# Performance work log

Hardware: AMD Instinct MI355X
Metric: run time of the kernel (lower is better)

The kernel has to match this reference:

```python
import jax, jax.numpy as jnp
import numpy as np

D_IN = 1024
D_OUT = 1024


def setup_inputs() -> dict:
    key = jax.random.key(0)
    kx, kq, kk, kv = jax.random.split(key, 4)
    x = jax.random.normal(kx, (4, 2048, D_IN), dtype=jnp.float32)
    s = 1.0 / np.sqrt(D_IN)
    # Linear weights stored torch-style as [d_out, d_in]
    W_q = jax.random.uniform(kq, (D_OUT, D_IN), jnp.float32, -s, s)
    W_k = jax.random.uniform(kk, (D_OUT, D_IN), jnp.float32, -s, s)
    W_v = jax.random.uniform(kv, (D_OUT, D_IN), jnp.float32, -s, s)
    return {"x": x, "W_q": W_q, "W_k": W_k, "W_v": W_v}


def reference(x, W_q, W_k, W_v):
    b, n, _ = x.shape
    q = jnp.einsum('bnd,od->bno', x, W_q)
    k = jnp.einsum('bnd,od->bno', x, W_k)
    v = jnp.einsum('bnd,od->bno', x, W_v)
    scores = jnp.einsum('bqo,bko->bqk', q, k)  # [b, n, n]
    causal = jnp.triu(jnp.ones((n, n), dtype=bool), k=1)
    scores = jnp.where(causal, -jnp.inf, scores)
    w = jax.nn.softmax(scores / jnp.sqrt(jnp.asarray(k.shape[-1], scores.dtype)), axis=-1)
    # dropout prob = 0.0 -> identity
    return jnp.einsum('bqk,bko->bqo', w, v)
```

## Files before the change

### kernel.cpp

```cpp
#include <hip/hip_runtime.h>
#include <hip/hip_bf16.h>

typedef unsigned int uint32;
typedef unsigned short ushort_t;

typedef __bf16 bf16x8 __attribute__((ext_vector_type(8)));
typedef float f32x4 __attribute__((ext_vector_type(4)));

__device__ __forceinline__ ushort_t f2bf(float f) {
    uint32 u = __float_as_uint(f);
    u += 0x7fffu + ((u >> 16) & 1u);
    return (ushort_t)(u >> 16);
}
__device__ __forceinline__ float bf2f(ushort_t h) {
    return __uint_as_float(((uint32)h) << 16);
}

union U16 { int4 v; ushort_t u[8]; };

__device__ __forceinline__ void gll16(const ushort_t* g, ushort_t* l) {
    __builtin_amdgcn_global_load_lds(
        (const __attribute__((address_space(1))) unsigned int*)g,
        (__attribute__((address_space(3))) unsigned int*)l, 16, 0, 0);
}

#define SBAR() __builtin_amdgcn_s_barrier()
#define VM0()  asm volatile("s_waitcnt vmcnt(0)" ::: "memory")
#define VM1()  asm volatile("s_waitcnt vmcnt(1)" ::: "memory")
#define VM2()  asm volatile("s_waitcnt vmcnt(2)" ::: "memory")

__device__ __forceinline__ int frag3(int r, int kk) {
    return r * 32 + ((((kk >> 3) ^ ((r >> 1) & 3))) << 3);
}

template<int NT>
__device__ __forceinline__ void gemm256_bk32(
    const ushort_t* __restrict__ A, int lda,
    const ushort_t* __restrict__ B, int ldb,
    ushort_t* lds, f32x4 acc[4][4])
{
    const int tid = threadIdx.x;
    const int lane = tid & 63, wid = tid >> 6;
    const int wm = wid >> 2, wn = wid & 3;
    const int l15 = lane & 15, kk = (lane >> 4) * 8;
    const int srow = tid >> 2;
    const int sc4 = (tid & 3) ^ ((tid >> 3) & 3);

    #define STAGE3(G, ldg, X, op)                                            \
        gll16(&(G)[(size_t)srow * (ldg) + (X) * 32 + sc4 * 8],               \
              &lds[(((X) % 3) * 2 + (op)) * 8192 + tid * 8])

    STAGE3(A, lda, 0, 0);
    STAGE3(B, ldb, 0, 1);
    if (NT > 1) { STAGE3(B, ldb, 1, 1); VM1(); } else { VM0(); }
    SBAR();

    for (int t = 0; t < NT; ++t) {
        const ushort_t* Ab = lds + (t % 3) * 16384;
        const ushort_t* Bb = Ab + 8192;
        if (t + 1 < NT) STAGE3(A, lda, t + 1, 0);
        if (t + 2 < NT) STAGE3(B, ldb, t + 2, 1);
        bf16x8 af[4], bfr[4];
#pragma unroll
        for (int m = 0; m < 4; ++m)
            af[m] = *(const bf16x8*)&Ab[frag3(wm * 64 + m * 16 + l15, kk)];
#pragma unroll
        for (int n = 0; n < 4; ++n)
            bfr[n] = *(const bf16x8*)&Bb[frag3(wn * 64 + n * 16 + l15, kk)];
#pragma unroll
        for (int m = 0; m < 4; ++m)
#pragma unroll
            for (int n = 0; n < 4; ++n)
                acc[m][n] = __builtin_amdgcn_mfma_f32_16x16x32_bf16(
                    af[m], bfr[n], acc[m][n], 0, 0, 0);
        if (t + 1 < NT) {
            if (t + 2 < NT) VM1(); else VM0();
            SBAR();
        }
    }
    #undef STAGE3
}

__device__ __forceinline__ void gemm128_bk32(
    const ushort_t* __restrict__ A, int lda,
    const ushort_t* __restrict__ B, int ldb,
    ushort_t* lds, int NT, f32x4 acc[4][4])
{
    const int tid = threadIdx.x;
    const int lane = tid & 63, wid = tid >> 6;
    const int wm = wid >> 1, wn = wid & 1;
    const int l15 = lane & 15, kk = (lane >> 4) * 8;

    #define STG128(G, ldg, X, op) do {                                       \
        _Pragma("unroll")                                                    \
        for (int i = 0; i < 2; ++i) {                                        \
            int c = i * 256 + tid;                   \
            int row = c >> 2;                                                \
            int slot = (c & 3) ^ ((row >> 1) & 3);                           \
            gll16(&(G)[(size_t)row * (ldg) + (X) * 32 + slot * 8],           \
                  &lds[(((X) % 3) * 2 + (op)) * 4096 + c * 8]);              \
        } } while (0)

    STG128(A, lda, 0, 0);
    STG128(B, ldb, 0, 1);
    if (NT > 1) { STG128(B, ldb, 1, 1); VM2(); } else { VM0(); }
    SBAR();

    for (int t = 0; t < NT; ++t) {
        const ushort_t* Ab = lds + (t % 3) * 8192;
        const ushort_t* Bb = Ab + 4096;
        if (t + 1 < NT) STG128(A, lda, t + 1, 0);
        if (t + 2 < NT) STG128(B, ldb, t + 2, 1);
        bf16x8 af[4], bfr[4];
#pragma unroll
        for (int m = 0; m < 4; ++m)
            af[m] = *(const bf16x8*)&Ab[frag3(wm * 64 + m * 16 + l15, kk)];
#pragma unroll
        for (int n = 0; n < 4; ++n)
            bfr[n] = *(const bf16x8*)&Bb[frag3(wn * 64 + n * 16 + l15, kk)];
#pragma unroll
        for (int m = 0; m < 4; ++m)
#pragma unroll
            for (int n = 0; n < 4; ++n)
                acc[m][n] = __builtin_amdgcn_mfma_f32_16x16x32_bf16(
                    af[m], bfr[n], acc[m][n], 0, 0, 0);
        if (t + 1 < NT) {
            if (t + 2 < NT) VM2(); else VM0();
            SBAR();
        }
    }
    #undef STG128
}

__global__ __launch_bounds__(256) void conv_x(
    const float* __restrict__ X, const float* __restrict__ Wv,
    ushort_t* __restrict__ Xb, ushort_t* __restrict__ BmatV)
{
    int gb = blockIdx.x;
    const float* src;
    ushort_t* dst;
    if (gb < 4096) {
        size_t base = ((size_t)gb * 256 + threadIdx.x) * 8;
        src = X + base; dst = Xb + base;
    } else {
        size_t base = ((size_t)(gb - 4096) * 256 + threadIdx.x) * 8;
        src = Wv + base; dst = BmatV + base;
    }
    float4 f0 = *(const float4*)src;
    float4 f1 = *(const float4*)(src + 4);
    U16 o;
    o.u[0] = f2bf(f0.x); o.u[1] = f2bf(f0.y); o.u[2] = f2bf(f0.z); o.u[3] = f2bf(f0.w);
    o.u[4] = f2bf(f1.x); o.u[5] = f2bf(f1.y); o.u[6] = f2bf(f1.z); o.u[7] = f2bf(f1.w);
    *(int4*)dst = o.v;
}

__global__ __launch_bounds__(256) void convT_w(
    const float* __restrict__ Wq, const float* __restrict__ Wk,
    ushort_t* __restrict__ WqT, ushort_t* __restrict__ WkT)
{
    __shared__ ushort_t ts[64][72];
    const float* W = blockIdx.z ? Wk : Wq;
    ushort_t* Dt = blockIdx.z ? WkT : WqT;
    const int o0 = blockIdx.x * 64, d0 = blockIdx.y * 64;
    const int tid = threadIdx.x;
    const int row = tid >> 2, q = tid & 3;
#pragma unroll
    for (int c4 = 0; c4 < 4; ++c4) {
        float4 f = *(const float4*)&W[(size_t)(o0 + row) * 1024 + d0 + q * 16 + c4 * 4];
        ts[row][q * 16 + c4 * 4 + 0] = f2bf(f.x);
        ts[row][q * 16 + c4 * 4 + 1] = f2bf(f.y);
        ts[row][q * 16 + c4 * 4 + 2] = f2bf(f.z);
        ts[row][q * 16 + c4 * 4 + 3] = f2bf(f.w);
    }
    __syncthreads();
#pragma unroll
    for (int i = 0; i < 2; ++i) {
        int c = tid + 256 * i;
        int drow = c >> 3, ocol8 = c & 7;
        U16 vv;
#pragma unroll
        for (int j = 0; j < 8; ++j) vv.u[j] = ts[ocol8 * 8 + j][drow];
        *(int4*)&Dt[(size_t)(d0 + drow) * 1024 + o0 + ocol8 * 8] = vv.v;
    }
}

__global__ __launch_bounds__(256) void mt_gemm(
    const ushort_t* __restrict__ WkT, const ushort_t* __restrict__ WqT,
    ushort_t* __restrict__ Bmat)
{
    __shared__ __align__(16) ushort_t lds[24576];
    const int bm = blockIdx.y, bn = blockIdx.x;
    const int tid = threadIdx.x;
    f32x4 acc[4][4] = {};
    gemm128_bk32(WkT + (size_t)bm * 128 * 1024, 1024,
                 WqT + (size_t)bn * 128 * 1024, 1024, lds, 32, acc);
    ushort_t* Dst = Bmat + (size_t)bm * 128 * 1024 + bn * 128;
    const int lane = tid & 63, wid = tid >> 6;
    const int wr = wid >> 1, wc = wid & 1;
#pragma unroll
    for (int m = 0; m < 4; ++m)
#pragma unroll
        for (int n = 0; n < 4; ++n)
#pragma unroll
            for (int j = 0; j < 4; ++j) {
                int row = wr * 64 + m * 16 + (lane >> 4) * 4 + j;
                int col = wc * 64 + n * 16 + (lane & 15);
                Dst[(size_t)row * 1024 + col] = f2bf(acc[m][n][j]);
            }
}

__global__ __launch_bounds__(1024) void t1v_gemm256(
    const ushort_t* __restrict__ Xb, const ushort_t* __restrict__ Bmat,
    ushort_t* __restrict__ T1, ushort_t* __restrict__ V)
{
    __shared__ __align__(16) ushort_t lds[49152];
    const int id = blockIdx.x;
    const int xcd = id & 7, l = id >> 3;
    const int bm = xcd * 4 + (l >> 3);
    const int bn = l & 7;
    f32x4 acc[4][4] = {};
    gemm256_bk32<32>(Xb + (size_t)bm * 256 * 1024, 1024,
                     Bmat + (size_t)bn * 256 * 1024, 1024, lds, acc);
    ushort_t* Dst = ((bn < 4) ? T1 : V)
                  + (size_t)bm * 256 * 1024 + (bn & 3) * 256;
    const int tid = threadIdx.x, lane = tid & 63, wid = tid >> 6;
    const int wm = wid >> 2, wn = wid & 3;
#pragma unroll
    for (int m = 0; m < 4; ++m)
#pragma unroll
        for (int n = 0; n < 4; ++n)
#pragma unroll
            for (int j = 0; j < 4; ++j) {
                int row = wm * 64 + m * 16 + (lane >> 4) * 4 + j;
                int col = wn * 64 + n * 16 + (lane & 15);
                Dst[(size_t)row * 1024 + col] = f2bf(acc[m][n][j]);
            }
}

__global__ __launch_bounds__(1024) void scores_gemm256(
    const ushort_t* __restrict__ T1, const ushort_t* __restrict__ Xb,
    ushort_t* __restrict__ P,
    const ushort_t* __restrict__ V, ushort_t* __restrict__ Vt)
{
    __shared__ __align__(16) ushort_t lds[49152];
    const int id = blockIdx.x;
    const int xcd = id & 7, l = id >> 3;
    const int b = xcd >> 1, h = xcd & 1;
    const int bm = 4 * h + (l >> 3);
    const int bn = l & 7;
    const int tid = threadIdx.x;
    if (bn > bm) {
        ushort_t (*ts)[72] = (ushort_t(*)[72])lds;
        const ushort_t* Vb = V + (size_t)b * 2048 * 1024;
        ushort_t* Vtb = Vt + (size_t)b * 1024 * 2048;
        const int rank = bn * (bn - 1) / 2 + bm;
        for (int t = rank; t < 512; t += 28) {
            int k0 = (t >> 4) * 64, d0 = (t & 15) * 64;
            __syncthreads();
            if (tid < 512) {
                int row = tid >> 3, col8 = tid & 7;
                U16 vv;
                vv.v = *(const int4*)&Vb[(size_t)(k0 + row) * 1024 + d0 + col8 * 8];
#pragma unroll
                for (int j = 0; j < 8; ++j) ts[row][col8 * 8 + j] = vv.u[j];
            }
            __syncthreads();
            if (tid < 512) {
                int drow = tid >> 3, kcol8 = tid & 7;
                U16 vv;
#pragma unroll
                for (int j = 0; j < 8; ++j) vv.u[j] = ts[kcol8 * 8 + j][drow];
                *(int4*)&Vtb[(size_t)(d0 + drow) * 2048 + k0 + kcol8 * 8] = vv.v;
            }
        }
        return;
    }
    f32x4 acc[4][4] = {};
    gemm256_bk32<32>(T1 + (size_t)b * 2048 * 1024 + (size_t)bm * 256 * 1024, 1024,
                     Xb + (size_t)b * 2048 * 1024 + (size_t)bn * 256 * 1024, 1024,
                     lds, acc);
    ushort_t* Pb = P + (size_t)b * 2048 * 2048 + (size_t)bm * 256 * 2048 + bn * 256;
    const int lane = tid & 63, wid = tid >> 6;
    const int wm = wid >> 2, wn = wid & 3;
#pragma unroll
    for (int m = 0; m < 4; ++m)
#pragma unroll
        for (int n = 0; n < 4; ++n)
#pragma unroll
            for (int j = 0; j < 4; ++j) {
                int row = wm * 64 + m * 16 + (lane >> 4) * 4 + j;
                int col = wn * 64 + n * 16 + (lane & 15);
                Pb[(size_t)row * 2048 + col] = f2bf(acc[m][n][j] * 0.03125f);
            }
}

__global__ __launch_bounds__(256) void softmax_rows(ushort_t* __restrict__ P)
{
    const int q = blockIdx.x, b = blockIdx.y;
    ushort_t* row = P + ((size_t)b * 2048 + q) * 2048;
    const int tid = threadIdx.x;
    const int kmax = ((q >> 7) + 1) * 128;
    const bool active = tid * 8 < kmax;
    float v[8];
    float m = -3.0e38f;
    if (active) {
        U16 in;
        in.v = *(const int4*)&row[tid * 8];
#pragma unroll
        for (int j = 0; j < 8; ++j) {
            int k = tid * 8 + j;
            float s = bf2f(in.u[j]);
            v[j] = (k <= q) ? s : -3.0e38f;
            m = fmaxf(m, v[j]);
        }
    } else {
#pragma unroll
        for (int j = 0; j < 8; ++j) v[j] = -3.0e38f;
    }
#pragma unroll
    for (int off = 32; off >= 1; off >>= 1) m = fmaxf(m, __shfl_xor(m, off));
    __shared__ float red[4];
    if ((tid & 63) == 0) red[tid >> 6] = m;
    __syncthreads();
    m = fmaxf(fmaxf(red[0], red[1]), fmaxf(red[2], red[3]));
    float e[8], s = 0.f;
#pragma unroll
    for (int j = 0; j < 8; ++j) {
        e[j] = (v[j] > -1.0e38f) ? __expf(v[j] - m) : 0.f;
        s += e[j];
    }
#pragma unroll
    for (int off = 32; off >= 1; off >>= 1) s += __shfl_xor(s, off);
    __syncthreads();
    if ((tid & 63) == 0) red[tid >> 6] = s;
    __syncthreads();
    s = red[0] + red[1] + red[2] + red[3];
    float inv = 1.f / s;
    if (active) {
        U16 outv;
#pragma unroll
        for (int j = 0; j < 8; ++j) outv.u[j] = f2bf(e[j] * inv);
        *(int4*)&row[tid * 8] = outv.v;
    }
}

__global__ __launch_bounds__(256) void pv_gemm(
    const ushort_t* __restrict__ P, const ushort_t* __restrict__ Vt,
    float* __restrict__ O)
{
    __shared__ __align__(16) ushort_t lds[24576];
    const int L = blockIdx.x;
    int b, bm, bn;
    if (L < 256) {
        int c = L >> 4;
        b = c >> 3; bn = c & 7; bm = 15 - (L & 15);
    } else {
        int L2 = L - 256;
        int c = L2 >> 4;
        b = 2 + (c >> 3); bn = c & 7; bm = L2 & 15;
    }
    const int tid = threadIdx.x;
    const ushort_t* A = P + (size_t)b * 2048 * 2048 + (size_t)bm * 128 * 2048;
    const ushort_t* Bm = Vt + (size_t)b * 1024 * 2048 + (size_t)bn * 128 * 2048;
    f32x4 acc[4][4] = {};
    const int NT = (bm + 1) * 4;
    gemm128_bk32(A, 2048, Bm, 2048, lds, NT, acc);
    float* Ob = O + (size_t)b * 2048 * 1024 + (size_t)bm * 128 * 1024 + bn * 128;
    const int lane = tid & 63, wid = tid >> 6;
    const int wr = wid >> 1, wc = wid & 1;
#pragma unroll
    for (int m = 0; m < 4; ++m)
#pragma unroll
        for (int n = 0; n < 4; ++n)
#pragma unroll
            for (int j = 0; j < 4; ++j) {
                int row = wr * 64 + m * 16 + (lane >> 4) * 4 + j;
                int col = wc * 64 + n * 16 + (lane & 15);
                Ob[(size_t)row * 1024 + col] = acc[m][n][j];
            }
}

extern "C" void kernel_launch(void* const* d_in, const int* in_sizes, int n_in,
                              void* d_out, int out_size, void* d_ws, size_t ws_size,
                              hipStream_t stream) {
    const float* x  = (const float*)d_in[0];
    const float* Wq = (const float*)d_in[1];
    const float* Wk = (const float*)d_in[2];
    const float* Wv = (const float*)d_in[3];
    float* out = (float*)d_out;
    ushort_t* ws = (ushort_t*)d_ws;
    const size_t M1 = (size_t)1024 * 1024;
    ushort_t* P    = ws;
    ushort_t* WqT  = ws;
    ushort_t* WkT  = ws + M1;
    ushort_t* Bmat = ws + 2 * M1;
    ushort_t* Xb   = ws + 16 * M1;
    ushort_t* T1   = ws + 24 * M1;
    ushort_t* V    = ws + 32 * M1;
    ushort_t* Vt   = ws + 40 * M1;

    conv_x<<<dim3(4096 + 512), 256, 0, stream>>>(x, Wv, Xb, Bmat + M1);
    convT_w<<<dim3(16, 16, 2), 256, 0, stream>>>(Wq, Wk, WqT, WkT);
    mt_gemm<<<dim3(8, 8), 256, 0, stream>>>(WkT, WqT, Bmat);
    t1v_gemm256<<<dim3(256), 1024, 0, stream>>>(Xb, Bmat, T1, V);
    scores_gemm256<<<dim3(256), 1024, 0, stream>>>(T1, Xb, P, V, Vt);
    softmax_rows<<<dim3(2048, 4), 256, 0, stream>>>(P);
    pv_gemm<<<dim3(512), 256, 0, stream>>>(P, Vt, out);
}
```

Baseline: 148.3 us.

## Fuse causal softmax into PV GEMM with online softmax and merge conversion kernels

Removes the separate softmax pass over the bf16 score matrix and applies an online softmax inside the PV GEMM. Each tile computes running row max and sum across the 16-lane fragment group, rescales accumulators when the max grows, and normalizes at the end. This saves a full read and write of the score matrix plus one launch, at the cost of extra ALU, shuffle and exp work inside the MFMA loop. The two fp32-to-bf16 conversion kernels are also merged into one launch.

```diff
diff --git a/kernel.cpp b/kernel.cpp
--- a/kernel.cpp
+++ b/kernel.cpp
@@ -17,6 +17,7 @@
 }
 
 union U16 { int4 v; ushort_t u[8]; };
+union UB8 { bf16x8 v; ushort_t u[8]; };
 
 __device__ __forceinline__ void gll16(const ushort_t* g, ushort_t* l) {
     __builtin_amdgcn_global_load_lds(
@@ -94,7 +95,7 @@
     #define STG128(G, ldg, X, op) do {                                       \
         _Pragma("unroll")                                                    \
         for (int i = 0; i < 2; ++i) {                                        \
-            int c = i * 256 + tid;                   \
+            int c = i * 256 + tid;                                           \
             int row = c >> 2;                                                \
             int slot = (c & 3) ^ ((row >> 1) & 3);                           \
             gll16(&(G)[(size_t)row * (ldg) + (X) * 32 + slot * 8],           \
@@ -132,37 +133,39 @@
     #undef STG128
 }
 
-__global__ __launch_bounds__(256) void conv_x(
-    const float* __restrict__ X, const float* __restrict__ Wv,
-    ushort_t* __restrict__ Xb, ushort_t* __restrict__ BmatV)
-{
-    int gb = blockIdx.x;
-    const float* src;
-    ushort_t* dst;
-    if (gb < 4096) {
-        size_t base = ((size_t)gb * 256 + threadIdx.x) * 8;
-        src = X + base; dst = Xb + base;
-    } else {
-        size_t base = ((size_t)(gb - 4096) * 256 + threadIdx.x) * 8;
-        src = Wv + base; dst = BmatV + base;
-    }
-    float4 f0 = *(const float4*)src;
-    float4 f1 = *(const float4*)(src + 4);
-    U16 o;
-    o.u[0] = f2bf(f0.x); o.u[1] = f2bf(f0.y); o.u[2] = f2bf(f0.z); o.u[3] = f2bf(f0.w);
-    o.u[4] = f2bf(f1.x); o.u[5] = f2bf(f1.y); o.u[6] = f2bf(f1.z); o.u[7] = f2bf(f1.w);
-    *(int4*)dst = o.v;
-}
-
-__global__ __launch_bounds__(256) void convT_w(
-    const float* __restrict__ Wq, const float* __restrict__ Wk,
+__global__ __launch_bounds__(256) void conv_all(
+    const float* __restrict__ X,  const float* __restrict__ Wq,
+    const float* __restrict__ Wk, const float* __restrict__ Wv,
+    ushort_t* __restrict__ Xb, ushort_t* __restrict__ BmatV,
     ushort_t* __restrict__ WqT, ushort_t* __restrict__ WkT)
 {
     __shared__ ushort_t ts[64][72];
-    const float* W = blockIdx.z ? Wk : Wq;
-    ushort_t* Dt = blockIdx.z ? WkT : WqT;
-    const int o0 = blockIdx.x * 64, d0 = blockIdx.y * 64;
-    const int tid = threadIdx.x;
+    const int gb = blockIdx.x;
+    const int tid = threadIdx.x;
+    if (gb < 4608) {
+        const float* src;
+        ushort_t* dst;
+        if (gb < 4096) {
+            size_t base = ((size_t)gb * 256 + tid) * 8;
+            src = X + base; dst = Xb + base;
+        } else {
+            size_t base = ((size_t)(gb - 4096) * 256 + tid) * 8;
+            src = Wv + base; dst = BmatV + base;
+        }
+        float4 f0 = *(const float4*)src;
+        float4 f1 = *(const float4*)(src + 4);
+        U16 o;
+        o.u[0] = f2bf(f0.x); o.u[1] = f2bf(f0.y); o.u[2] = f2bf(f0.z); o.u[3] = f2bf(f0.w);
+        o.u[4] = f2bf(f1.x); o.u[5] = f2bf(f1.y); o.u[6] = f2bf(f1.z); o.u[7] = f2bf(f1.w);
+        *(int4*)dst = o.v;
+        return;
+    }
+    const int t2 = gb - 4608;
+    const int z = t2 >> 8;
+    const int bx = t2 & 15, by = (t2 >> 4) & 15;
+    const float* W = z ? Wk : Wq;
+    ushort_t* Dt = z ? WkT : WqT;
+    const int o0 = bx * 64, d0 = by * 64;
     const int row = tid >> 2, q = tid & 3;
 #pragma unroll
     for (int c4 = 0; c4 < 4; ++c4) {
@@ -294,58 +297,8 @@
             }
 }
 
-__global__ __launch_bounds__(256) void softmax_rows(ushort_t* __restrict__ P)
-{
-    const int q = blockIdx.x, b = blockIdx.y;
-    ushort_t* row = P + ((size_t)b * 2048 + q) * 2048;
-    const int tid = threadIdx.x;
-    const int kmax = ((q >> 7) + 1) * 128;
-    const bool active = tid * 8 < kmax;
-    float v[8];
-    float m = -3.0e38f;
-    if (active) {
-        U16 in;
-        in.v = *(const int4*)&row[tid * 8];
-#pragma unroll
-        for (int j = 0; j < 8; ++j) {
-            int k = tid * 8 + j;
-            float s = bf2f(in.u[j]);
-            v[j] = (k <= q) ? s : -3.0e38f;
-            m = fmaxf(m, v[j]);
-        }
-    } else {
-#pragma unroll
-        for (int j = 0; j < 8; ++j) v[j] = -3.0e38f;
-    }
-#pragma unroll
-    for (int off = 32; off >= 1; off >>= 1) m = fmaxf(m, __shfl_xor(m, off));
-    __shared__ float red[4];
-    if ((tid & 63) == 0) red[tid >> 6] = m;
-    __syncthreads();
-    m = fmaxf(fmaxf(red[0], red[1]), fmaxf(red[2], red[3]));
-    float e[8], s = 0.f;
-#pragma unroll
-    for (int j = 0; j < 8; ++j) {
-        e[j] = (v[j] > -1.0e38f) ? __expf(v[j] - m) : 0.f;
-        s += e[j];
-    }
-#pragma unroll
-    for (int off = 32; off >= 1; off >>= 1) s += __shfl_xor(s, off);
-    __syncthreads();
-    if ((tid & 63) == 0) red[tid >> 6] = s;
-    __syncthreads();
-    s = red[0] + red[1] + red[2] + red[3];
-    float inv = 1.f / s;
-    if (active) {
-        U16 outv;
-#pragma unroll
-        for (int j = 0; j < 8; ++j) outv.u[j] = f2bf(e[j] * inv);
-        *(int4*)&row[tid * 8] = outv.v;
-    }
-}
-
-__global__ __launch_bounds__(256) void pv_gemm(
-    const ushort_t* __restrict__ P, const ushort_t* __restrict__ Vt,
+__global__ __launch_bounds__(256) void pv_fused(
+    const ushort_t* __restrict__ S, const ushort_t* __restrict__ Vt,
     float* __restrict__ O)
 {
     __shared__ __align__(16) ushort_t lds[24576];
@@ -360,24 +313,119 @@
         b = 2 + (c >> 3); bn = c & 7; bm = L2 & 15;
     }
     const int tid = threadIdx.x;
-    const ushort_t* A = P + (size_t)b * 2048 * 2048 + (size_t)bm * 128 * 2048;
+    const int lane = tid & 63, wid = tid >> 6;
+    const int wm = wid >> 1, wn = wid & 1;
+    const int l15 = lane & 15, kk = (lane >> 4) * 8;
+    const ushort_t* A = S + (size_t)b * 2048 * 2048 + (size_t)bm * 128 * 2048;
     const ushort_t* Bm = Vt + (size_t)b * 1024 * 2048 + (size_t)bn * 128 * 2048;
+    const int NT = (bm + 1) * 4;
+
     f32x4 acc[4][4] = {};
-    const int NT = (bm + 1) * 4;
-    gemm128_bk32(A, 2048, Bm, 2048, lds, NT, acc);
+    float m_run[4] = {-3.0e38f, -3.0e38f, -3.0e38f, -3.0e38f};
+    float l_run[4] = {0.f, 0.f, 0.f, 0.f};
+    const int qrow_base = bm * 128 + wm * 64 + l15;
+
+    #define STGF(G, ldg, X, op) do {                                         \
+        _Pragma("unroll")                                                    \
+        for (int i = 0; i < 2; ++i) {                                        \
+            int c = i * 256 + tid;                                           \
+            int row = c >> 2;                                                \
+            int slot = (c & 3) ^ ((row >> 1) & 3);                           \
+            gll16(&(G)[(size_t)row * (ldg) + (X) * 32 + slot * 8],           \
+                  &lds[(((X) % 3) * 2 + (op)) * 4096 + c * 8]);              \
+        } } while (0)
+
+    STGF(A, 2048, 0, 0);
+    STGF(Bm, 2048, 0, 1);
+    if (NT > 1) { STGF(Bm, 2048, 1, 1); VM2(); } else { VM0(); }
+    SBAR();
+
+    for (int t = 0; t < NT; ++t) {
+        const ushort_t* Ab = lds + (t % 3) * 8192;
+        const ushort_t* Bb = Ab + 4096;
+        if (t + 1 < NT) STGF(A, 2048, t + 1, 0);
+        if (t + 2 < NT) STGF(Bm, 2048, t + 2, 1);
+        UB8 af[4];
+        bf16x8 bfr[4], pa[4];
+#pragma unroll
+        for (int m = 0; m < 4; ++m)
+            af[m].v = *(const bf16x8*)&Ab[frag3(wm * 64 + m * 16 + l15, kk)];
+#pragma unroll
+        for (int n = 0; n < 4; ++n)
+            bfr[n] = *(const bf16x8*)&Bb[frag3(wn * 64 + n * 16 + l15, kk)];
+
+        const bool maskT = (t >= NT - 4);
+        const int kbase = t * 32 + kk;
+#pragma unroll
+        for (int m = 0; m < 4; ++m) {
+            float sv[8];
+#pragma unroll
+            for (int e = 0; e < 8; ++e) sv[e] = bf2f(af[m].u[e]);
+            if (maskT) {
+                int dk = (qrow_base + m * 16) - kbase;
+#pragma unroll
+                for (int e = 0; e < 8; ++e)
+                    if (e > dk) sv[e] = -3.0e38f;
+            }
+            float tm = sv[0];
+#pragma unroll
+            for (int e = 1; e < 8; ++e) tm = fmaxf(tm, sv[e]);
+            tm = fmaxf(tm, __shfl_xor(tm, 16));
+            tm = fmaxf(tm, __shfl_xor(tm, 32));
+            const bool grew = (tm > m_run[m]);
+            float mn = grew ? tm : m_run[m];
+            float ls = 0.f;
+            UB8 pu;
+#pragma unroll
+            for (int e = 0; e < 8; ++e) {
+                float p = __expf(sv[e] - mn);
+                ls += p;
+                pu.u[e] = f2bf(p);
+            }
+            pa[m] = pu.v;
+            ls += __shfl_xor(ls, 16);
+            ls += __shfl_xor(ls, 32);
+            if (__any(grew)) {
+                float rs = __expf(m_run[m] - mn);
+                l_run[m] = l_run[m] * rs + ls;
+                m_run[m] = mn;
+#pragma unroll
+                for (int j = 0; j < 4; ++j) {
+                    float sj = __shfl(rs, (lane >> 4) * 4 + j);
+#pragma unroll
+                    for (int n = 0; n < 4; ++n) acc[m][n][j] *= sj;
+                }
+            } else {
+                l_run[m] += ls;
+            }
+        }
+#pragma unroll
+        for (int m = 0; m < 4; ++m)
+#pragma unroll
+            for (int n = 0; n < 4; ++n)
+                acc[m][n] = __builtin_amdgcn_mfma_f32_16x16x32_bf16(
+                    pa[m], bfr[n], acc[m][n], 0, 0, 0);
+        if (t + 1 < NT) {
+            if (t + 2 < NT) VM2(); else VM0();
+            SBAR();
+        }
+    }
+    #undef STGF
+
     float* Ob = O + (size_t)b * 2048 * 1024 + (size_t)bm * 128 * 1024 + bn * 128;
-    const int lane = tid & 63, wid = tid >> 6;
-    const int wr = wid >> 1, wc = wid & 1;
 #pragma unroll
     for (int m = 0; m < 4; ++m)
 #pragma unroll
-        for (int n = 0; n < 4; ++n)
-#pragma unroll
-            for (int j = 0; j < 4; ++j) {
-                int row = wr * 64 + m * 16 + (lane >> 4) * 4 + j;
-                int col = wc * 64 + n * 16 + (lane & 15);
-                Ob[(size_t)row * 1024 + col] = acc[m][n][j];
-            }
+        for (int j = 0; j < 4; ++j) {
+            float lj = __shfl(l_run[m], (lane >> 4) * 4 + j);
+            float inv = 1.f / lj;
+            int row = wm * 64 + m * 16 + (lane >> 4) * 4 + j;
+#pragma unroll
+            for (int n = 0; n < 4; ++n) {
+                int col = wn * 64 + n * 16 + (lane & 15);
+                Ob[(size_t)row * 1024 + col] = acc[m][n][j] * inv;
+            }
+        }
 }
 
 extern "C" void kernel_launch(void* const* d_in, const int* in_sizes, int n_in,
@@ -399,11 +447,10 @@
     ushort_t* V    = ws + 32 * M1;
     ushort_t* Vt   = ws + 40 * M1;
 
-    conv_x<<<dim3(4096 + 512), 256, 0, stream>>>(x, Wv, Xb, Bmat + M1);
-    convT_w<<<dim3(16, 16, 2), 256, 0, stream>>>(Wq, Wk, WqT, WkT);
+    conv_all<<<dim3(4608 + 512), 256, 0, stream>>>(x, Wq, Wk, Wv,
+                                                   Xb, Bmat + M1, WqT, WkT);
     mt_gemm<<<dim3(8, 8), 256, 0, stream>>>(WkT, WqT, Bmat);
     t1v_gemm256<<<dim3(256), 1024, 0, stream>>>(Xb, Bmat, T1, V);
     scores_gemm256<<<dim3(256), 1024, 0, stream>>>(T1, Xb, P, V, Vt);
-    softmax_rows<<<dim3(2048, 4), 256, 0, stream>>>(P);
-    pv_gemm<<<dim3(512), 256, 0, stream>>>(P, Vt, out);
-}
+    pv_fused<<<dim3(512), 256, 0, stream>>>(P, Vt, out);
+}
```

Result: slower. 228.0 us (+53.7%).
